# Optimization experiments

Hardware: AMD Instinct MI355X
Metric: run time of the kernel (lower is better)

Reference implementation:

```python
import jax, jax.numpy as jnp
import numpy as np

EMBED = 1024
HEADS = 16
HEAD_DIM = EMBED // HEADS
SCALE = HEAD_DIM ** (-0.5)
LN_EPS = 1e-5


def setup_inputs() -> dict:
    key = jax.random.key(0)
    ks = jax.random.split(key, 8)
    B, N = 2, 2048
    s = EMBED ** -0.5
    return {
        "x": jax.random.normal(ks[0], (B, N, EMBED), dtype=jnp.float32),
        "ln_w": jnp.ones((EMBED,), jnp.float32),
        "ln_b": jnp.zeros((EMBED,), jnp.float32),
        "Wq": jax.random.normal(ks[1], (EMBED, EMBED), jnp.float32) * s,
        "Wk": jax.random.normal(ks[2], (EMBED, EMBED), jnp.float32) * s,
        "Wv": jax.random.normal(ks[3], (EMBED, EMBED), jnp.float32) * s,
        "Wo": jax.random.normal(ks[4], (EMBED, EMBED), jnp.float32) * s,
        "bo": jnp.zeros((EMBED,), jnp.float32),
    }


def reference(x, ln_w, ln_b, Wq, Wk, Wv, Wo, bo):
    residual = x
    # LayerNorm (pre-norm)
    mu = jnp.mean(x, axis=-1, keepdims=True)
    var = jnp.mean(jnp.square(x - mu), axis=-1, keepdims=True)
    xn = (x - mu) * jax.lax.rsqrt(var + LN_EPS) * ln_w + ln_b

    B, N, _ = xn.shape
    q = (xn @ Wq.T).reshape(B, N, HEADS, HEAD_DIM).transpose(0, 2, 1, 3)  # b h n d
    k = (xn @ Wk.T).reshape(B, N, HEADS, HEAD_DIM).transpose(0, 2, 1, 3)
    v = (xn @ Wv.T).reshape(B, N, HEADS, HEAD_DIM).transpose(0, 2, 1, 3)

    dots = jnp.einsum('bhqd,bhkd->bhqk', q, k) * SCALE
    causal = jnp.tril(jnp.ones((N, N), dtype=bool))
    dots = jnp.where(causal, dots, -jnp.inf)
    attn = jax.nn.softmax(dots, axis=-1)
    out = jnp.einsum('bhqk,bhkd->bhqd', attn, v)
    out = out.transpose(0, 2, 1, 3).reshape(B, N, EMBED)
    # dropout is identity in eval mode
    return residual + out @ Wo.T + bo
```

## Files before the change

### kernel.cpp

```cpp
#include <hip/hip_runtime.h>

#define E 1024
#define NSEQ 2048
#define HEADS 16
#define HD 64

typedef unsigned short u16;
typedef short short8 __attribute__((ext_vector_type(8)));
typedef float f32x4 __attribute__((ext_vector_type(4)));

template<bool B> struct BC { static constexpr bool v = B; };

#define GLOAD_LDS16(gp, lp)                                        \
    __builtin_amdgcn_global_load_lds(                              \
        (const __attribute__((address_space(1))) void*)(gp),       \
        (__attribute__((address_space(3))) void*)(lp), 16, 0, 0)

__device__ __forceinline__ u16 f2bf(float f) {
    union { float f; unsigned u; } v; v.f = f;
    unsigned r = v.u + 0x7fffu + ((v.u >> 16) & 1u);
    return (u16)(r >> 16);
}

__device__ __forceinline__ unsigned cvt_pk_bf16(float lo, float hi) {
    unsigned r;
    asm("v_cvt_pk_bf16_f32 %0, %1, %2" : "=v"(r) : "v"(lo), "v"(hi));
    return r;
}

__device__ __forceinline__ f32x4 mfma16(short8 a, short8 b, f32x4 c) {
    return __builtin_amdgcn_mfma_f32_16x16x32_bf16(a, b, c, 0, 0, 0);
}

__global__ __launch_bounds__(256) void convw_k(
    const float* __restrict__ Wq, const float* __restrict__ Wk,
    const float* __restrict__ Wv, const float* __restrict__ Wo,
    u16* __restrict__ out)
{
    const unsigned i = (blockIdx.x * 256u + threadIdx.x) * 4u;
    const unsigned m = i >> 20;
    const float* src = (m == 0) ? Wq : (m == 1) ? Wk : (m == 2) ? Wv : Wo;
    const float4 v = *(const float4*)(src + (i & 0xFFFFFu));
    *(uint2*)(out + i) = make_uint2(
        ((unsigned)f2bf(v.x)) | (((unsigned)f2bf(v.y)) << 16),
        ((unsigned)f2bf(v.z)) | (((unsigned)f2bf(v.w)) << 16));
}

__global__ __launch_bounds__(256) void ln_fwd(
    const float* __restrict__ X, const float* __restrict__ w,
    const float* __restrict__ bb, u16* __restrict__ xn)
{
    const int row = blockIdx.x, tid = threadIdx.x;
    const int lane = tid & 63, wave = tid >> 6;
    const float4 v = ((const float4*)(X + (size_t)row * E))[tid];
    float s = v.x + v.y + v.z + v.w;
    float s2 = v.x * v.x + v.y * v.y + v.z * v.z + v.w * v.w;
#pragma unroll
    for (int off = 1; off < 64; off <<= 1) {
        s += __shfl_xor(s, off);
        s2 += __shfl_xor(s2, off);
    }
    __shared__ float red[8];
    if (lane == 0) { red[wave] = s; red[4 + wave] = s2; }
    __syncthreads();
    s = red[0] + red[1] + red[2] + red[3];
    s2 = red[4] + red[5] + red[6] + red[7];
    const float mu = s * (1.f / 1024.f);
    float var = s2 * (1.f / 1024.f) - mu * mu;
    var = fmaxf(var, 0.f);
    const float rs = rsqrtf(var + 1e-5f);
    const float4 wv = ((const float4*)w)[tid];
    const float4 bv = ((const float4*)bb)[tid];
    u16 o0 = f2bf((v.x - mu) * rs * wv.x + bv.x);
    u16 o1 = f2bf((v.y - mu) * rs * wv.y + bv.y);
    u16 o2 = f2bf((v.z - mu) * rs * wv.z + bv.z);
    u16 o3 = f2bf((v.w - mu) * rs * wv.w + bv.w);
    *(uint2*)(xn + (size_t)row * E + tid * 4) =
        make_uint2(((unsigned)o0) | (((unsigned)o1) << 16),
                   ((unsigned)o2) | (((unsigned)o3) << 16));
}

__global__ __launch_bounds__(256) void vtrans(
    const u16* __restrict__ Vb, u16* __restrict__ VT)
{
    __shared__ u16 tl[64][65];
    const int t = threadIdx.x;
    const int ntile = blockIdx.x, bh = blockIdx.y;
    const int b = bh >> 4, h = bh & 15;
    const int n0 = ntile * 64;
    {
        const int nl = t >> 2;
        const u16* src = Vb + ((size_t)b * NSEQ + n0 + nl) * E + h * 64;
#pragma unroll
        for (int u = 0; u < 2; ++u) {
            const int d0 = (t & 3) * 16 + u * 8;
            short8 v = *(const short8*)(src + d0);
#pragma unroll
            for (int j = 0; j < 8; ++j) tl[nl][d0 + j] = (u16)v[j];
        }
    }
    __syncthreads();
    {
        const int d = t >> 2, nc = (t & 3) * 16;
        u16* dst = VT + ((size_t)bh * 64 + d) * NSEQ + n0 + nc;
#pragma unroll
        for (int u = 0; u < 2; ++u) {
            short8 o;
#pragma unroll
            for (int j = 0; j < 8; ++j) o[j] = (short)tl[nc + u * 8 + j][d];
            *(short8*)(dst + u * 8) = o;
        }
    }
}

template<int MODE>
__global__ __launch_bounds__(256) void gemm_nt(
    const u16* __restrict__ A, const u16* __restrict__ Wbase,
    u16* __restrict__ outb, float* __restrict__ outf,
    const float* __restrict__ resid, const float* __restrict__ bias)
{
    __shared__ __align__(16) unsigned char As[128 * 128];
    __shared__ __align__(16) unsigned char Bs[128 * 128];
    const int tid = threadIdx.x;
    const int lane = tid & 63, wave = tid >> 6;
    const int l15 = lane & 15, l4 = lane >> 4;
    const int wm = wave >> 1, wn = wave & 1;
    const int nt = blockIdx.x, mt = blockIdx.y, z = blockIdx.z;
    const u16* Bw = Wbase + (size_t)z * (E * (size_t)E);

    const int lrow8 = lane >> 3;
    const int lchunk = (lane & 7) ^ lrow8;
    const u16* gA = A + (size_t)(mt * 128 + lrow8) * E + lchunk * 8;
    const u16* gB = Bw + (size_t)(nt * 128 + lrow8) * E + lchunk * 8;

    f32x4 acc[4][4] = {};

    for (int kt = 0; kt < 16; ++kt) {
#pragma unroll
        for (int i = 0; i < 4; ++i) {
            const int rb = (i * 4 + wave) * 8;
            GLOAD_LDS16(gA + (size_t)rb * E + kt * 64, As + rb * 128);
            GLOAD_LDS16(gB + (size_t)rb * E + kt * 64, Bs + rb * 128);
        }
        __syncthreads();
#pragma unroll
        for (int ks = 0; ks < 2; ++ks) {
            short8 af[4], bfr[4];
#pragma unroll
            for (int i = 0; i < 4; ++i) {
                int ra = wm * 64 + i * 16 + l15;
                af[i] = *(const short8*)(As + ra * 128 + ((ks * 64 + l4 * 16) ^ ((ra & 7) << 4)));
                int rb2 = wn * 64 + i * 16 + l15;
                bfr[i] = *(const short8*)(Bs + rb2 * 128 + ((ks * 64 + l4 * 16) ^ ((rb2 & 7) << 4)));
            }
#pragma unroll
            for (int i = 0; i < 4; ++i)
#pragma unroll
                for (int j = 0; j < 4; ++j)
                    acc[i][j] = mfma16(af[i], bfr[j], acc[i][j]);
        }
        __syncthreads();
    }

    const int orow0 = mt * 128 + wm * 64, ocol0 = nt * 128 + wn * 64;
    if (MODE == 0) {
        u16* outz = outb + (size_t)z * (4096 * (size_t)E);
        const float osc = (z == 0) ? 0.18033688f : 1.0f;
#pragma unroll
        for (int i = 0; i < 4; ++i)
#pragma unroll
            for (int j = 0; j < 4; ++j)
#pragma unroll
                for (int r = 0; r < 4; ++r) {
                    int row = orow0 + i * 16 + l4 * 4 + r;
                    int col = ocol0 + j * 16 + l15;
                    outz[(size_t)row * E + col] = f2bf(acc[i][j][r] * osc);
                }
    } else {
#pragma unroll
        for (int i = 0; i < 4; ++i)
#pragma unroll
            for (int j = 0; j < 4; ++j)
#pragma unroll
                for (int r = 0; r < 4; ++r) {
                    int row = orow0 + i * 16 + l4 * 4 + r;
                    int col = ocol0 + j * 16 + l15;
                    size_t idx = (size_t)row * E + col;
                    outf[idx] = acc[i][j][r] + resid[idx] + bias[col];
                }
    }
}

__global__ __launch_bounds__(256) void attn_fwd(
    const u16* __restrict__ Q, const u16* __restrict__ K,
    const u16* __restrict__ VT, u16* __restrict__ O)
{
    __shared__ __align__(16) unsigned char Kls[2 * 16384];
    __shared__ __align__(16) unsigned char Ps[4 * 4096];
    const int tid = threadIdx.x, lane = tid & 63, wave = tid >> 6;
    const int sub = wave >> 1, par = wave & 1;
    const int l15 = lane & 15, l4 = lane >> 4;
    const int h = blockIdx.x, jg = blockIdx.y, b = blockIdx.z;
    const size_t bbase = (size_t)b * NSEQ * E + h * HD;
    const u16* vt = VT + ((size_t)(b * 16 + h) * 64) * NSEQ;

    unsigned char* Pw = Ps + wave * 4096;
    const int srowK = lane >> 3, kchunk = (lane & 7) ^ srowK;

    int koff[4][2];
#pragma unroll
    for (int kvt = 0; kvt < 4; ++kvt) {
        const int kr = par * 64 + kvt * 16 + l15;
#pragma unroll
        for (int ks = 0; ks < 2; ++ks)
            koff[kvt][ks] = kr * 128 + ((ks * 64 + l4 * 16) ^ ((kr & 7) << 4));
    }
    int pwo[2][4];
#pragma unroll
    for (int qt = 0; qt < 2; ++qt) {
        const int pr = qt * 16 + l15;
#pragma unroll
        for (int kvt = 0; kvt < 4; ++kvt)
            pwo[qt][kvt] = pr * 128 + ((kvt * 32 + l4 * 8) ^ ((l15 & 7) << 4));
    }
    int pro[2][2];
#pragma unroll
    for (int ks2 = 0; ks2 < 2; ++ks2) {
        const int cb = (ks2 * 64 + l4 * 16) ^ ((l15 & 7) << 4);
        pro[ks2][0] = l15 * 128 + cb;
        pro[ks2][1] = (16 + l15) * 128 + cb;
    }
    int vgo[2][4];
#pragma unroll
    for (int ks2 = 0; ks2 < 2; ++ks2)
#pragma unroll
        for (int dt = 0; dt < 4; ++dt)
            vgo[ks2][dt] = (dt * 16 + l15) * NSEQ + par * 64 + ks2 * 32 + l4 * 8;

    auto stage = [&](int t, int buf) {
        const u16* Kg = K + bbase + (size_t)(t * 128) * E;
        unsigned char* kd = Kls + buf * 16384 + wave * 1024;
#pragma unroll
        for (int i = 0; i < 4; ++i)
            GLOAD_LDS16(Kg + (size_t)(wave * 8 + i * 32 + srowK) * E + kchunk * 8, kd + i * 4096);
    };

    auto run_strip = [&](int jj) {
        const int qw0 = jj * 64 + sub * 32;
        const int R = (jj >> 1) + 1;

        short8 aq[2][2];
#pragma unroll
        for (int qt = 0; qt < 2; ++qt)
#pragma unroll
            for (int ks = 0; ks < 2; ++ks)
                aq[qt][ks] = *(const short8*)(Q + bbase + (size_t)(qw0 + qt * 16 + l15) * E + ks * 32 + l4 * 8);

        f32x4 accO[2][4] = {};
        float mrow[2] = {-5e29f, -5e29f};
        float lrow[2] = {0.f, 0.f};

        short8 vf[2][4];
#pragma unroll
        for (int ks2 = 0; ks2 < 2; ++ks2)
#pragma unroll
            for (int dt = 0; dt < 4; ++dt)
                vf[ks2][dt] = *(const short8*)(vt + vgo[ks2][dt]);

        stage(0, 0);
        __syncthreads();

        auto step = [&](int t, auto mc) {
            constexpr bool MASK = decltype(mc)::v;
            const int buf = t & 1;
            if (t + 1 < R) stage(t + 1, buf ^ 1);
            const unsigned char* Kc = Kls + buf * 16384;

            f32x4 s[2][4] = {};
            __builtin_amdgcn_s_setprio(1);
#pragma unroll
            for (int kvt = 0; kvt < 4; ++kvt)
#pragma unroll
                for (int ks = 0; ks < 2; ++ks) {
                    short8 kfr = *(const short8*)(Kc + koff[kvt][ks]);
                    s[0][kvt] = mfma16(kfr, aq[0][ks], s[0][kvt]);
                    s[1][kvt] = mfma16(kfr, aq[1][ks], s[1][kvt]);
                }
            __builtin_amdgcn_s_setprio(0);

            if constexpr (MASK) {
#pragma unroll
                for (int qt = 0; qt < 2; ++qt) {
                    const int qg = qw0 + qt * 16 + l15;
#pragma unroll
                    for (int kvt = 0; kvt < 4; ++kvt)
#pragma unroll
                        for (int r = 0; r < 4; ++r) {
                            int kvg = t * 128 + par * 64 + kvt * 16 + l4 * 4 + r;
                            if (kvg > qg) s[qt][kvt][r] = -1e30f;
                        }
                }
            }

#pragma unroll
            for (int qt = 0; qt < 2; ++qt) {
                float m0 = fmaxf(fmaxf(s[qt][0][0], s[qt][0][1]), fmaxf(s[qt][0][2], s[qt][0][3]));
                float m1 = fmaxf(fmaxf(s[qt][1][0], s[qt][1][1]), fmaxf(s[qt][1][2], s[qt][1][3]));
                float m2 = fmaxf(fmaxf(s[qt][2][0], s[qt][2][1]), fmaxf(s[qt][2][2], s[qt][2][3]));
                float m3 = fmaxf(fmaxf(s[qt][3][0], s[qt][3][1]), fmaxf(s[qt][3][2], s[qt][3][3]));
                float pm = fmaxf(fmaxf(m0, m1), fmaxf(m2, m3));
                if (__any(pm > mrow[qt] + 8.f)) {
                    pm = fmaxf(pm, __shfl_xor(pm, 16));
                    pm = fmaxf(pm, __shfl_xor(pm, 32));
                    const float mn = fmaxf(mrow[qt], pm);
                    const float sc = exp2f(mrow[qt] - mn);
                    mrow[qt] = mn;
                    lrow[qt] *= sc;
#pragma unroll
                    for (int r = 0; r < 4; ++r) {
                        float scv = __shfl(sc, l4 * 4 + r);
#pragma unroll
                        for (int dt = 0; dt < 4; ++dt) accO[qt][dt][r] *= scv;
                    }
                }
#pragma unroll
                for (int kvt = 0; kvt < 4; ++kvt) {
                    float p0 = exp2f(s[qt][kvt][0] - mrow[qt]);
                    float p1 = exp2f(s[qt][kvt][1] - mrow[qt]);
                    float p2 = exp2f(s[qt][kvt][2] - mrow[qt]);
                    float p3 = exp2f(s[qt][kvt][3] - mrow[qt]);
                    lrow[qt] += (p0 + p1) + (p2 + p3);
                    uint2 pk = make_uint2(cvt_pk_bf16(p0, p1), cvt_pk_bf16(p2, p3));
                    *(uint2*)(Pw + pwo[qt][kvt]) = pk;
                }
            }

            __builtin_amdgcn_s_setprio(1);
#pragma unroll
            for (int ks2 = 0; ks2 < 2; ++ks2) {
                short8 pf0 = *(const short8*)(Pw + pro[ks2][0]);
                short8 pf1 = *(const short8*)(Pw + pro[ks2][1]);
#pragma unroll
                for (int dt = 0; dt < 4; ++dt) {
                    accO[0][dt] = mfma16(pf0, vf[ks2][dt], accO[0][dt]);
                    accO[1][dt] = mfma16(pf1, vf[ks2][dt], accO[1][dt]);
                }
            }
            __builtin_amdgcn_s_setprio(0);

            if (t + 1 < R) {
                const u16* vg = vt + (t + 1) * 128;
#pragma unroll
                for (int ks2 = 0; ks2 < 2; ++ks2)
#pragma unroll
                    for (int dt = 0; dt < 4; ++dt)
                        vf[ks2][dt] = *(const short8*)(vg + vgo[ks2][dt]);
            }
            __syncthreads();
        };

        for (int t = 0; t + 1 < R; ++t) step(t, BC<false>{});
        step(R - 1, BC<true>{});

        f32x4* Mg = (f32x4*)Kls;
        if (par == 1) {
            f32x4 hd;
            hd[0] = mrow[0]; hd[1] = mrow[1]; hd[2] = lrow[0]; hd[3] = lrow[1];
            Mg[(sub * 9) * 64 + lane] = hd;
#pragma unroll
            for (int qt = 0; qt < 2; ++qt)
#pragma unroll
                for (int dt = 0; dt < 4; ++dt)
                    Mg[(sub * 9 + 1 + qt * 4 + dt) * 64 + lane] = accO[qt][dt];
        }
        __syncthreads();
        if (par == 0) {
            f32x4 hd = Mg[(sub * 9) * 64 + lane];
            float scA[2], scB[2];
#pragma unroll
            for (int qt = 0; qt < 2; ++qt) {
                const float mB = hd[qt], lB = hd[2 + qt];
                const float ms = fmaxf(mrow[qt], mB);
                scA[qt] = exp2f(mrow[qt] - ms);
                scB[qt] = exp2f(mB - ms);
                lrow[qt] = lrow[qt] * scA[qt] + lB * scB[qt];
            }
#pragma unroll
            for (int qt = 0; qt < 2; ++qt)
#pragma unroll
                for (int r = 0; r < 4; ++r) {
                    float sa = __shfl(scA[qt], l4 * 4 + r);
                    float sb = __shfl(scB[qt], l4 * 4 + r);
#pragma unroll
                    for (int dt = 0; dt < 4; ++dt) {
                        f32x4 ob = Mg[(sub * 9 + 1 + qt * 4 + dt) * 64 + lane];
                        accO[qt][dt][r] = accO[qt][dt][r] * sa + ob[r] * sb;
                    }
                }
            float linv[2];
#pragma unroll
            for (int qt = 0; qt < 2; ++qt) {
                float tl2 = lrow[qt];
                tl2 += __shfl_xor(tl2, 16);
                tl2 += __shfl_xor(tl2, 32);
                linv[qt] = 1.f / tl2;
            }
#pragma unroll
            for (int rt = 0; rt < 2; ++rt)
#pragma unroll
                for (int r = 0; r < 4; ++r) {
                    float lq = __shfl(linv[rt], l4 * 4 + r);
                    const int qg = qw0 + rt * 16 + l4 * 4 + r;
#pragma unroll
                    for (int dt = 0; dt < 4; ++dt)
                        O[bbase + (size_t)qg * E + dt * 16 + l15] = f2bf(accO[rt][dt][r] * lq);
                }
        }
        __syncthreads();
    };

    run_strip(jg);
    run_strip(31 - jg);
}

extern "C" void kernel_launch(void* const* d_in, const int* in_sizes, int n_in,
                              void* d_out, int out_size, void* d_ws, size_t ws_size,
                              hipStream_t stream)
{
    const float* x    = (const float*)d_in[0];
    const float* ln_w = (const float*)d_in[1];
    const float* ln_b = (const float*)d_in[2];
    const float* Wq   = (const float*)d_in[3];
    const float* Wk   = (const float*)d_in[4];
    const float* Wv   = (const float*)d_in[5];
    const float* Wo   = (const float*)d_in[6];
    const float* bo   = (const float*)d_in[7];
    float* out = (float*)d_out;

    u16* ws  = (u16*)d_ws;
    u16* Wbf = ws;
    u16* xn  = Wbf + (size_t)4 * 1024 * 1024;
    u16* Qb  = xn + (size_t)4096 * 1024;
    u16* Kb  = Qb + (size_t)4096 * 1024;
    u16* Vb  = Kb + (size_t)4096 * 1024;
    u16* Ob  = Vb + (size_t)4096 * 1024;
    u16* VT  = xn;

    convw_k<<<dim3(4096), dim3(256), 0, stream>>>(Wq, Wk, Wv, Wo, Wbf);
    ln_fwd<<<dim3(4096), dim3(256), 0, stream>>>(x, ln_w, ln_b, xn);
    gemm_nt<0><<<dim3(8, 32, 3), dim3(256), 0, stream>>>(
        xn, Wbf, Qb, nullptr, nullptr, nullptr);
    vtrans<<<dim3(32, 32), dim3(256), 0, stream>>>(Vb, VT);
    attn_fwd<<<dim3(16, 16, 2), dim3(256), 0, stream>>>(Qb, Kb, VT, Ob);
    gemm_nt<1><<<dim3(8, 32, 1), dim3(256), 0, stream>>>(
        Ob, Wbf + (size_t)3 * 1024 * 1024, nullptr, out, x, bo);
}
```

Measured before the change: 126.6 us.

## Fuse weight-convert with LayerNorm, one strip per attention block, double-buffer V

Result: slower. 153.8 us (+21.4%).

```diff
diff --git a/kernel.cpp b/kernel.cpp
--- a/kernel.cpp
+++ b/kernel.cpp
@@ -32,25 +32,23 @@
     return __builtin_amdgcn_mfma_f32_16x16x32_bf16(a, b, c, 0, 0, 0);
 }
 
-__global__ __launch_bounds__(256) void convw_k(
+__global__ __launch_bounds__(256) void prep_k(
     const float* __restrict__ Wq, const float* __restrict__ Wk,
     const float* __restrict__ Wv, const float* __restrict__ Wo,
-    u16* __restrict__ out)
+    const float* __restrict__ X, const float* __restrict__ w,
+    const float* __restrict__ bb, u16* __restrict__ Wbf, u16* __restrict__ xn)
 {
-    const unsigned i = (blockIdx.x * 256u + threadIdx.x) * 4u;
-    const unsigned m = i >> 20;
-    const float* src = (m == 0) ? Wq : (m == 1) ? Wk : (m == 2) ? Wv : Wo;
-    const float4 v = *(const float4*)(src + (i & 0xFFFFFu));
-    *(uint2*)(out + i) = make_uint2(
-        ((unsigned)f2bf(v.x)) | (((unsigned)f2bf(v.y)) << 16),
-        ((unsigned)f2bf(v.z)) | (((unsigned)f2bf(v.w)) << 16));
-}
-
-__global__ __launch_bounds__(256) void ln_fwd(
-    const float* __restrict__ X, const float* __restrict__ w,
-    const float* __restrict__ bb, u16* __restrict__ xn)
-{
-    const int row = blockIdx.x, tid = threadIdx.x;
+    if (blockIdx.x < 4096) {
+        const unsigned i = (blockIdx.x * 256u + threadIdx.x) * 4u;
+        const unsigned m = i >> 20;
+        const float* src = (m == 0) ? Wq : (m == 1) ? Wk : (m == 2) ? Wv : Wo;
+        const float4 v = *(const float4*)(src + (i & 0xFFFFFu));
+        *(uint2*)(Wbf + i) = make_uint2(
+            ((unsigned)f2bf(v.x)) | (((unsigned)f2bf(v.y)) << 16),
+            ((unsigned)f2bf(v.z)) | (((unsigned)f2bf(v.w)) << 16));
+        return;
+    }
+    const int row = blockIdx.x - 4096, tid = threadIdx.x;
     const int lane = tid & 63, wave = tid >> 6;
     const float4 v = ((const float4*)(X + (size_t)row * E))[tid];
     float s = v.x + v.y + v.z + v.w;
@@ -200,7 +198,8 @@
     const int tid = threadIdx.x, lane = tid & 63, wave = tid >> 6;
     const int sub = wave >> 1, par = wave & 1;
     const int l15 = lane & 15, l4 = lane >> 4;
-    const int h = blockIdx.x, jg = blockIdx.y, b = blockIdx.z;
+    const int h = blockIdx.x, y = blockIdx.y, b = blockIdx.z;
+    const int jj = b ? (31 - (int)y) : (int)y;
     const size_t bbase = (size_t)b * NSEQ * E + h * HD;
     const u16* vt = VT + ((size_t)(b * 16 + h) * 64) * NSEQ;
 
@@ -245,182 +244,179 @@
             GLOAD_LDS16(Kg + (size_t)(wave * 8 + i * 32 + srowK) * E + kchunk * 8, kd + i * 4096);
     };
 
-    auto run_strip = [&](int jj) {
-        const int qw0 = jj * 64 + sub * 32;
-        const int R = (jj >> 1) + 1;
-
-        short8 aq[2][2];
-#pragma unroll
-        for (int qt = 0; qt < 2; ++qt)
-#pragma unroll
-            for (int ks = 0; ks < 2; ++ks)
-                aq[qt][ks] = *(const short8*)(Q + bbase + (size_t)(qw0 + qt * 16 + l15) * E + ks * 32 + l4 * 8);
-
-        f32x4 accO[2][4] = {};
-        float mrow[2] = {-5e29f, -5e29f};
-        float lrow[2] = {0.f, 0.f};
-
-        short8 vf[2][4];
-#pragma unroll
-        for (int ks2 = 0; ks2 < 2; ++ks2)
-#pragma unroll
-            for (int dt = 0; dt < 4; ++dt)
-                vf[ks2][dt] = *(const short8*)(vt + vgo[ks2][dt]);
-
-        stage(0, 0);
-        __syncthreads();
-
-        auto step = [&](int t, auto mc) {
-            constexpr bool MASK = decltype(mc)::v;
-            const int buf = t & 1;
-            if (t + 1 < R) stage(t + 1, buf ^ 1);
-            const unsigned char* Kc = Kls + buf * 16384;
-
-            f32x4 s[2][4] = {};
-            __builtin_amdgcn_s_setprio(1);
-#pragma unroll
-            for (int kvt = 0; kvt < 4; ++kvt)
-#pragma unroll
-                for (int ks = 0; ks < 2; ++ks) {
-                    short8 kfr = *(const short8*)(Kc + koff[kvt][ks]);
-                    s[0][kvt] = mfma16(kfr, aq[0][ks], s[0][kvt]);
-                    s[1][kvt] = mfma16(kfr, aq[1][ks], s[1][kvt]);
+    const int qw0 = jj * 64 + sub * 32;
+    const int R = (jj >> 1) + 1;
+
+    short8 aq[2][2];
+#pragma unroll
+    for (int qt = 0; qt < 2; ++qt)
+#pragma unroll
+        for (int ks = 0; ks < 2; ++ks)
+            aq[qt][ks] = *(const short8*)(Q + bbase + (size_t)(qw0 + qt * 16 + l15) * E + ks * 32 + l4 * 8);
+
+    f32x4 accO[2][4] = {};
+    float mrow[2] = {-5e29f, -5e29f};
+    float lrow[2] = {0.f, 0.f};
+
+    short8 vfA[2][4], vfB[2][4];
+#pragma unroll
+    for (int ks2 = 0; ks2 < 2; ++ks2)
+#pragma unroll
+        for (int dt = 0; dt < 4; ++dt)
+            vfA[ks2][dt] = *(const short8*)(vt + vgo[ks2][dt]);
+
+    stage(0, 0);
+    __syncthreads();
+
+    auto step = [&](int t, short8 (&vcur)[2][4], short8 (&vnxt)[2][4], auto mc) {
+        constexpr bool MASK = decltype(mc)::v;
+        const int buf = t & 1;
+        if (t + 1 < R) {
+            stage(t + 1, buf ^ 1);
+            const u16* vg = vt + (t + 1) * 128;
+#pragma unroll
+            for (int ks2 = 0; ks2 < 2; ++ks2)
+#pragma unroll
+                for (int dt = 0; dt < 4; ++dt)
+                    vnxt[ks2][dt] = *(const short8*)(vg + vgo[ks2][dt]);
+        }
+        const unsigned char* Kc = Kls + buf * 16384;
+
+        f32x4 s[2][4] = {};
+        __builtin_amdgcn_s_setprio(1);
+#pragma unroll
+        for (int kvt = 0; kvt < 4; ++kvt)
+#pragma unroll
+            for (int ks = 0; ks < 2; ++ks) {
+                short8 kfr = *(const short8*)(Kc + koff[kvt][ks]);
+                s[0][kvt] = mfma16(kfr, aq[0][ks], s[0][kvt]);
+                s[1][kvt] = mfma16(kfr, aq[1][ks], s[1][kvt]);
+            }
+        __builtin_amdgcn_s_setprio(0);
+
+        if constexpr (MASK) {
+#pragma unroll
+            for (int qt = 0; qt < 2; ++qt) {
+                const int qg = qw0 + qt * 16 + l15;
+#pragma unroll
+                for (int kvt = 0; kvt < 4; ++kvt)
+#pragma unroll
+                    for (int r = 0; r < 4; ++r) {
+                        int kvg = t * 128 + par * 64 + kvt * 16 + l4 * 4 + r;
+                        if (kvg > qg) s[qt][kvt][r] = -1e30f;
+                    }
+            }
+        }
+
+#pragma unroll
+        for (int qt = 0; qt < 2; ++qt) {
+            float m0 = fmaxf(fmaxf(s[qt][0][0], s[qt][0][1]), fmaxf(s[qt][0][2], s[qt][0][3]));
+            float m1 = fmaxf(fmaxf(s[qt][1][0], s[qt][1][1]), fmaxf(s[qt][1][2], s[qt][1][3]));
+            float m2 = fmaxf(fmaxf(s[qt][2][0], s[qt][2][1]), fmaxf(s[qt][2][2], s[qt][2][3]));
+            float m3 = fmaxf(fmaxf(s[qt][3][0], s[qt][3][1]), fmaxf(s[qt][3][2], s[qt][3][3]));
+            float pm = fmaxf(fmaxf(m0, m1), fmaxf(m2, m3));
+            if (__any(pm > mrow[qt] + 8.f)) {
+                pm = fmaxf(pm, __shfl_xor(pm, 16));
+                pm = fmaxf(pm, __shfl_xor(pm, 32));
+                const float mn = fmaxf(mrow[qt], pm);
+                const float sc = exp2f(mrow[qt] - mn);
+                mrow[qt] = mn;
+                lrow[qt] *= sc;
+#pragma unroll
+                for (int r = 0; r < 4; ++r) {
+                    float scv = __shfl(sc, l4 * 4 + r);
+#pragma unroll
+                    for (int dt = 0; dt < 4; ++dt) accO[qt][dt][r] *= scv;
                 }
-            __builtin_amdgcn_s_setprio(0);
-
-            if constexpr (MASK) {
-#pragma unroll
-                for (int qt = 0; qt < 2; ++qt) {
-                    const int qg = qw0 + qt * 16 + l15;
-#pragma unroll
-                    for (int kvt = 0; kvt < 4; ++kvt)
-#pragma unroll
-                        for (int r = 0; r < 4; ++r) {
-                            int kvg = t * 128 + par * 64 + kvt * 16 + l4 * 4 + r;
-                            if (kvg > qg) s[qt][kvt][r] = -1e30f;
-                        }
-                }
-            }
-
-#pragma unroll
-            for (int qt = 0; qt < 2; ++qt) {
-                float m0 = fmaxf(fmaxf(s[qt][0][0], s[qt][0][1]), fmaxf(s[qt][0][2], s[qt][0][3]));
-                float m1 = fmaxf(fmaxf(s[qt][1][0], s[qt][1][1]), fmaxf(s[qt][1][2], s[qt][1][3]));
-                float m2 = fmaxf(fmaxf(s[qt][2][0], s[qt][2][1]), fmaxf(s[qt][2][2], s[qt][2][3]));
-                float m3 = fmaxf(fmaxf(s[qt][3][0], s[qt][3][1]), fmaxf(s[qt][3][2], s[qt][3][3]));
-                float pm = fmaxf(fmaxf(m0, m1), fmaxf(m2, m3));
-                if (__any(pm > mrow[qt] + 8.f)) {
-                    pm = fmaxf(pm, __shfl_xor(pm, 16));
-                    pm = fmaxf(pm, __shfl_xor(pm, 32));
-                    const float mn = fmaxf(mrow[qt], pm);
-                    const float sc = exp2f(mrow[qt] - mn);
-                    mrow[qt] = mn;
-                    lrow[qt] *= sc;
-#pragma unroll
-                    for (int r = 0; r < 4; ++r) {
-                        float scv = __shfl(sc, l4 * 4 + r);
-#pragma unroll
-                        for (int dt = 0; dt < 4; ++dt) accO[qt][dt][r] *= scv;
-                    }
-                }
-#pragma unroll
-                for (int kvt = 0; kvt < 4; ++kvt) {
-                    float p0 = exp2f(s[qt][kvt][0] - mrow[qt]);
-                    float p1 = exp2f(s[qt][kvt][1] - mrow[qt]);
-                    float p2 = exp2f(s[qt][kvt][2] - mrow[qt]);
-                    float p3 = exp2f(s[qt][kvt][3] - mrow[qt]);
-                    lrow[qt] += (p0 + p1) + (p2 + p3);
-                    uint2 pk = make_uint2(cvt_pk_bf16(p0, p1), cvt_pk_bf16(p2, p3));
-                    *(uint2*)(Pw + pwo[qt][kvt]) = pk;
-                }
-            }
-
-            __builtin_amdgcn_s_setprio(1);
-#pragma unroll
-            for (int ks2 = 0; ks2 < 2; ++ks2) {
-                short8 pf0 = *(const short8*)(Pw + pro[ks2][0]);
-                short8 pf1 = *(const short8*)(Pw + pro[ks2][1]);
-#pragma unroll
-                for (int dt = 0; dt < 4; ++dt) {
-                    accO[0][dt] = mfma16(pf0, vf[ks2][dt], accO[0][dt]);
-                    accO[1][dt] = mfma16(pf1, vf[ks2][dt], accO[1][dt]);
-                }
-            }
-            __builtin_amdgcn_s_setprio(0);
-
-            if (t + 1 < R) {
-                const u16* vg = vt + (t + 1) * 128;
-#pragma unroll
-                for (int ks2 = 0; ks2 < 2; ++ks2)
-#pragma unroll
-                    for (int dt = 0; dt < 4; ++dt)
-                        vf[ks2][dt] = *(const short8*)(vg + vgo[ks2][dt]);
-            }
-            __syncthreads();
-        };
-
-        for (int t = 0; t + 1 < R; ++t) step(t, BC<false>{});
-        step(R - 1, BC<true>{});
-
-        f32x4* Mg = (f32x4*)Kls;
-        if (par == 1) {
-            f32x4 hd;
-            hd[0] = mrow[0]; hd[1] = mrow[1]; hd[2] = lrow[0]; hd[3] = lrow[1];
-            Mg[(sub * 9) * 64 + lane] = hd;
-#pragma unroll
-            for (int qt = 0; qt < 2; ++qt)
-#pragma unroll
-                for (int dt = 0; dt < 4; ++dt)
-                    Mg[(sub * 9 + 1 + qt * 4 + dt) * 64 + lane] = accO[qt][dt];
-        }
-        __syncthreads();
-        if (par == 0) {
-            f32x4 hd = Mg[(sub * 9) * 64 + lane];
-            float scA[2], scB[2];
-#pragma unroll
-            for (int qt = 0; qt < 2; ++qt) {
-                const float mB = hd[qt], lB = hd[2 + qt];
-                const float ms = fmaxf(mrow[qt], mB);
-                scA[qt] = exp2f(mrow[qt] - ms);
-                scB[qt] = exp2f(mB - ms);
-                lrow[qt] = lrow[qt] * scA[qt] + lB * scB[qt];
-            }
-#pragma unroll
-            for (int qt = 0; qt < 2; ++qt)
-#pragma unroll
-                for (int r = 0; r < 4; ++r) {
-                    float sa = __shfl(scA[qt], l4 * 4 + r);
-                    float sb = __shfl(scB[qt], l4 * 4 + r);
-#pragma unroll
-                    for (int dt = 0; dt < 4; ++dt) {
-                        f32x4 ob = Mg[(sub * 9 + 1 + qt * 4 + dt) * 64 + lane];
-                        accO[qt][dt][r] = accO[qt][dt][r] * sa + ob[r] * sb;
-                    }
-                }
-            float linv[2];
-#pragma unroll
-            for (int qt = 0; qt < 2; ++qt) {
-                float tl2 = lrow[qt];
-                tl2 += __shfl_xor(tl2, 16);
-                tl2 += __shfl_xor(tl2, 32);
-                linv[qt] = 1.f / tl2;
-            }
-#pragma unroll
-            for (int rt = 0; rt < 2; ++rt)
-#pragma unroll
-                for (int r = 0; r < 4; ++r) {
-                    float lq = __shfl(linv[rt], l4 * 4 + r);
-                    const int qg = qw0 + rt * 16 + l4 * 4 + r;
-#pragma unroll
-                    for (int dt = 0; dt < 4; ++dt)
-                        O[bbase + (size_t)qg * E + dt * 16 + l15] = f2bf(accO[rt][dt][r] * lq);
-                }
-        }
+            }
+#pragma unroll
+            for (int kvt = 0; kvt < 4; ++kvt) {
+                float p0 = exp2f(s[qt][kvt][0] - mrow[qt]);
+                float p1 = exp2f(s[qt][kvt][1] - mrow[qt]);
+                float p2 = exp2f(s[qt][kvt][2] - mrow[qt]);
+                float p3 = exp2f(s[qt][kvt][3] - mrow[qt]);
+                lrow[qt] += (p0 + p1) + (p2 + p3);
+                uint2 pk = make_uint2(cvt_pk_bf16(p0, p1), cvt_pk_bf16(p2, p3));
+                *(uint2*)(Pw + pwo[qt][kvt]) = pk;
+            }
+        }
+
+        __builtin_amdgcn_s_setprio(1);
+#pragma unroll
+        for (int ks2 = 0; ks2 < 2; ++ks2) {
+            short8 pf0 = *(const short8*)(Pw + pro[ks2][0]);
+            short8 pf1 = *(const short8*)(Pw + pro[ks2][1]);
+#pragma unroll
+            for (int dt = 0; dt < 4; ++dt) {
+                accO[0][dt] = mfma16(pf0, vcur[ks2][dt], accO[0][dt]);
+                accO[1][dt] = mfma16(pf1, vcur[ks2][dt], accO[1][dt]);
+            }
+        }
+        __builtin_amdgcn_s_setprio(0);
         __syncthreads();
     };
 
-    run_strip(jg);
-    run_strip(31 - jg);
+    for (int t = 0; t + 1 < R; ++t) {
+        if (t & 1) step(t, vfB, vfA, BC<false>{});
+        else       step(t, vfA, vfB, BC<false>{});
+    }
+    if ((R - 1) & 1) step(R - 1, vfB, vfA, BC<true>{});
+    else             step(R - 1, vfA, vfB, BC<true>{});
+
+    f32x4* Mg = (f32x4*)Kls;
+    if (par == 1) {
+        f32x4 hd;
+        hd[0] = mrow[0]; hd[1] = mrow[1]; hd[2] = lrow[0]; hd[3] = lrow[1];
+        Mg[(sub * 9) * 64 + lane] = hd;
+#pragma unroll
+        for (int qt = 0; qt < 2; ++qt)
+#pragma unroll
+            for (int dt = 0; dt < 4; ++dt)
+                Mg[(sub * 9 + 1 + qt * 4 + dt) * 64 + lane] = accO[qt][dt];
+    }
+    __syncthreads();
+    if (par == 0) {
+        f32x4 hd = Mg[(sub * 9) * 64 + lane];
+        float scA[2], scB[2];
+#pragma unroll
+        for (int qt = 0; qt < 2; ++qt) {
+            const float mB = hd[qt], lB = hd[2 + qt];
+            const float ms = fmaxf(mrow[qt], mB);
+            scA[qt] = exp2f(mrow[qt] - ms);
+            scB[qt] = exp2f(mB - ms);
+            lrow[qt] = lrow[qt] * scA[qt] + lB * scB[qt];
+        }
+#pragma unroll
+        for (int qt = 0; qt < 2; ++qt)
+#pragma unroll
+            for (int r = 0; r < 4; ++r) {
+                float sa = __shfl(scA[qt], l4 * 4 + r);
+                float sb = __shfl(scB[qt], l4 * 4 + r);
+#pragma unroll
+                for (int dt = 0; dt < 4; ++dt) {
+                    f32x4 ob = Mg[(sub * 9 + 1 + qt * 4 + dt) * 64 + lane];
+                    accO[qt][dt][r] = accO[qt][dt][r] * sa + ob[r] * sb;
+                }
+            }
+        float linv[2];
+#pragma unroll
+        for (int qt = 0; qt < 2; ++qt) {
+            float tl2 = lrow[qt];
+            tl2 += __shfl_xor(tl2, 16);
+            tl2 += __shfl_xor(tl2, 32);
+            linv[qt] = 1.f / tl2;
+        }
+#pragma unroll
+        for (int rt = 0; rt < 2; ++rt)
+#pragma unroll
+            for (int r = 0; r < 4; ++r) {
+                float lq = __shfl(linv[rt], l4 * 4 + r);
+                const int qg = qw0 + rt * 16 + l4 * 4 + r;
+#pragma unroll
+                for (int dt = 0; dt < 4; ++dt)
+                    O[bbase + (size_t)qg * E + dt * 16 + l15] = f2bf(accO[rt][dt][r] * lq);
+            }
+    }
 }
 
 extern "C" void kernel_launch(void* const* d_in, const int* in_sizes, int n_in,
@@ -446,12 +442,11 @@
     u16* Ob  = Vb + (size_t)4096 * 1024;
     u16* VT  = xn;
 
-    convw_k<<<dim3(4096), dim3(256), 0, stream>>>(Wq, Wk, Wv, Wo, Wbf);
-    ln_fwd<<<dim3(4096), dim3(256), 0, stream>>>(x, ln_w, ln_b, xn);
+    prep_k<<<dim3(8192), dim3(256), 0, stream>>>(Wq, Wk, Wv, Wo, x, ln_w, ln_b, Wbf, xn);
     gemm_nt<0><<<dim3(8, 32, 3), dim3(256), 0, stream>>>(
         xn, Wbf, Qb, nullptr, nullptr, nullptr);
     vtrans<<<dim3(32, 32), dim3(256), 0, stream>>>(Vb, VT);
-    attn_fwd<<<dim3(16, 16, 2), dim3(256), 0, stream>>>(Qb, Kb, VT, Ob);
+    attn_fwd<<<dim3(16, 32, 2), dim3(256), 0, stream>>>(Qb, Kb, VT, Ob);
     gemm_nt<1><<<dim3(8, 32, 1), dim3(256), 0, stream>>>(
         Ob, Wbf + (size_t)3 * 1024 * 1024, nullptr, out, x, bo);
 }
```
